# Kernel tuning notes

Hardware: AMD Instinct MI355X
Metric: run time of the kernel (lower is better)

## Reference

```python
import jax, jax.numpy as jnp
import numpy as np

B, T, C = 4, 2048, 1024
H = 16
D = C // H  # head_dim = 64
SCALE = D ** -0.5


def setup_inputs() -> dict:
    key = jax.random.key(0)
    ks = jax.random.split(key, 5)
    x = jax.random.normal(ks[0], (B, T, C), dtype=jnp.float32)
    w_qkv = jax.random.normal(ks[1], (3 * C, C), dtype=jnp.float32) * (C ** -0.5)
    b_qkv = jnp.zeros((3 * C,), dtype=jnp.float32)
    w_proj = jax.random.normal(ks[2], (C, C), dtype=jnp.float32) * (C ** -0.5)
    b_proj = jnp.zeros((C,), dtype=jnp.float32)
    return {"x": x, "w_qkv": w_qkv, "b_qkv": b_qkv, "w_proj": w_proj, "b_proj": b_proj}


def reference(x, w_qkv, b_qkv, w_proj, b_proj):
    b, t, c = x.shape
    # fused qkv projection (torch Linear: x @ W.T + b)
    qkv = x @ w_qkv.T + b_qkv                      # [B, T, 3C]
    q, k, v = jnp.split(qkv, 3, axis=2)
    # [B, T, C] -> [B, H, T, D]
    q = q.reshape(b, t, H, D).transpose(0, 2, 1, 3)
    k = k.reshape(b, t, H, D).transpose(0, 2, 1, 3)
    v = v.reshape(b, t, H, D).transpose(0, 2, 1, 3)
    att = jnp.einsum('bhqd,bhkd->bhqk', q, k) * SCALE
    causal = jnp.tril(jnp.ones((t, t), dtype=bool))  # True = keep
    att = jnp.where(causal, att, -jnp.inf)
    att = jax.nn.softmax(att, axis=-1)
    out = jnp.einsum('bhqk,bhkd->bhqd', att, v)
    out = out.transpose(0, 2, 1, 3).reshape(b, t, c)
    return out @ w_proj.T + b_proj
```

## Files before the change

### kernel.cpp

```cpp
#include <hip/hip_runtime.h>

typedef unsigned short u16;
typedef __attribute__((ext_vector_type(8))) short short8;
typedef __attribute__((ext_vector_type(4))) float f32x4;
typedef __attribute__((ext_vector_type(16))) float f32x16;
typedef __attribute__((ext_vector_type(2))) unsigned uint2v;
typedef __attribute__((ext_vector_type(4))) unsigned u32x4;

#define AS1 __attribute__((address_space(1)))
#define AS3 __attribute__((address_space(3)))

constexpr int Bn = 4, Tn = 2048, Cn = 1024, Hn = 16, Dn = 64;
constexpr float SCL_LOG2E = 0.125f * 1.44269504088896f;

__device__ __forceinline__ u16 f2bf(float f) {
  union { float f; unsigned u; } v; v.f = f;
  unsigned r = v.u + 0x7FFFu + ((v.u >> 16) & 1u);
  return (u16)(r >> 16);
}

__device__ __forceinline__ unsigned cvtpk_bf16(float a, float b) {
  unsigned r;
  asm("v_cvt_pk_bf16_f32 %0, %1, %2" : "=v"(r) : "v"(a), "v"(b));
  return r;
}

__global__ void cast_f32_to_bf16(const float* __restrict__ in, u16* __restrict__ out, int n4) {
  int i = blockIdx.x * 256 + threadIdx.x;
  if (i >= n4) return;
  float4 v = ((const float4*)in)[i];
  ushort4 o;
  o.x = f2bf(v.x); o.y = f2bf(v.y); o.z = f2bf(v.z); o.w = f2bf(v.w);
  ((ushort4*)out)[i] = o;
}

template <typename OT>
__global__ __launch_bounds__(512) void gemm8(
    const u16* __restrict__ A, const u16* __restrict__ Bm,
    const float* __restrict__ bias, OT* __restrict__ C,
    int M, int N, int K, int nbn, int qcols, float qscale)
{
  __shared__ u16 As[2][128 * 64];
  __shared__ u16 Bs[2][128 * 64];

  const int tid = threadIdx.x;
  const int lane = tid & 63;
  const int w = tid >> 6;
  const int wm = w >> 2, wn = w & 3;
  const int l15 = lane & 15, lg = lane >> 4;

  const int nwg = gridDim.x;
  const int wg = (blockIdx.x & 7) * (nwg >> 3) + (blockIdx.x >> 3);
  const int m0 = (wg / nbn) * 128;
  const int n0 = (wg % nbn) * 128;
  const int NT = K >> 6;

  const int wrow = wm * 64;
  const int wcol = wn * 32;

  f32x4 acc[4][2] = {};

  auto stage_A = [&](int tt) {
    if (tt >= NT) return;
    const int bu = tt & 1;
#pragma unroll
    for (int it = 0; it < 2; ++it) {
      const int c = it * 512 + tid;
      const int row = c >> 3;
      const int cs = (c & 7) ^ (row & 7);
      const u16* g = A + (size_t)(m0 + row) * K + tt * 64 + cs * 8;
      __builtin_amdgcn_global_load_lds((const AS1 void*)g,
          (AS3 void*)(&As[bu][c * 8]), 16, 0, 0);
    }
  };
  auto stage_B = [&](int tt) {
    if (tt >= NT) return;
    const int bu = tt & 1;
#pragma unroll
    for (int it = 0; it < 2; ++it) {
      const int c = it * 512 + tid;
      const int row = c >> 3;
      const int cs = (c & 7) ^ (row & 7);
      const u16* g = Bm + (size_t)(n0 + row) * K + tt * 64 + cs * 8;
      __builtin_amdgcn_global_load_lds((const AS1 void*)g,
          (AS3 void*)(&Bs[bu][c * 8]), 16, 0, 0);
    }
  };

  auto readA = [&](int bu, int mh, short8 (*a)[2]) {
#pragma unroll
    for (int i = 0; i < 2; ++i)
#pragma unroll
      for (int ks = 0; ks < 2; ++ks) {
        const int ra = wrow + (mh * 2 + i) * 16 + l15;
        a[i][ks] = *(const short8*)(&As[bu][ra * 64 + (((ks * 4 + lg) ^ (ra & 7)) << 3)]);
      }
  };
  auto readB = [&](int bu, int nh, short8 (*b)[2]) {
#pragma unroll
    for (int ks = 0; ks < 2; ++ks) {
      const int rb = wcol + nh * 16 + l15;
      b[0][ks] = *(const short8*)(&Bs[bu][rb * 64 + (((ks * 4 + lg) ^ (rb & 7)) << 3)]);
    }
  };
  auto mmaq = [&](int mh, int nh, short8 (*a)[2], short8 (*b)[2]) {
    __builtin_amdgcn_s_setprio(1);
#pragma unroll
    for (int i = 0; i < 2; ++i)
#pragma unroll
      for (int ks = 0; ks < 2; ++ks)
        acc[mh * 2 + i][nh] = __builtin_amdgcn_mfma_f32_16x16x32_bf16(
            a[i][ks], b[0][ks], acc[mh * 2 + i][nh], 0, 0, 0);
    __builtin_amdgcn_s_setprio(0);
  };

  stage_A(0);
  stage_B(0);
  stage_A(1);
  asm volatile("s_waitcnt vmcnt(2)" ::: "memory");
  __builtin_amdgcn_sched_barrier(0);
  __builtin_amdgcn_s_barrier();

  for (int t = 0; t < NT; ++t) {
    const int bu = t & 1;
    short8 a0[2][2], a1[2][2], b0[1][2], b1[1][2];
    readA(bu, 0, a0);
    readB(bu, 0, b0);
    stage_B(t + 1);
    __builtin_amdgcn_s_barrier();
    mmaq(0, 0, a0, b0);
    __builtin_amdgcn_s_barrier();
    readB(bu, 1, b1);
    __builtin_amdgcn_s_barrier();
    mmaq(0, 1, a0, b1);
    __builtin_amdgcn_s_barrier();
    readA(bu, 1, a1);
    __builtin_amdgcn_s_barrier();
    mmaq(1, 1, a1, b1);
    __builtin_amdgcn_s_barrier();
    stage_A(t + 2);
    __builtin_amdgcn_s_barrier();
    mmaq(1, 0, a1, b0);
    if (t + 2 < NT) {
      asm volatile("s_waitcnt vmcnt(2)" ::: "memory");
      __builtin_amdgcn_sched_barrier(0);
    } else if (t + 1 < NT) {
      asm volatile("s_waitcnt vmcnt(0)" ::: "memory");
      __builtin_amdgcn_sched_barrier(0);
    }
    __builtin_amdgcn_s_barrier();
  }

  __syncthreads();
  if constexpr (__is_same(OT, u16)) {
    u16* bounce = &As[0][0];
#pragma unroll
    for (int i = 0; i < 4; ++i)
#pragma unroll
      for (int j = 0; j < 2; ++j) {
        const int colg = n0 + wcol + j * 16 + l15;
        const float sc = (colg < qcols) ? qscale : 1.0f;
        const float bv = bias[colg];
#pragma unroll
        for (int r = 0; r < 4; ++r)
          bounce[(wrow + i * 16 + lg * 4 + r) * 128 + wcol + j * 16 + l15] =
              f2bf((acc[i][j][r] + bv) * sc);
      }
    __syncthreads();
#pragma unroll
    for (int s = 0; s < 4; ++s) {
      const int u = s * 512 + tid;
      const int row = u >> 4, col = (u & 15) * 8;
      *(short8*)(C + (size_t)(m0 + row) * N + n0 + col) =
          *(const short8*)(&bounce[row * 128 + col]);
    }
  } else {
    float* bounce = (float*)&As[0][0];
#pragma unroll
    for (int cch = 0; cch < 2; ++cch) {
      if (wm == cch) {
#pragma unroll
        for (int i = 0; i < 4; ++i)
#pragma unroll
          for (int j = 0; j < 2; ++j) {
            const int colg = n0 + wcol + j * 16 + l15;
            const float bv = bias[colg];
#pragma unroll
            for (int r = 0; r < 4; ++r)
              bounce[(i * 16 + lg * 4 + r) * 128 + wcol + j * 16 + l15] =
                  acc[i][j][r] + bv;
          }
      }
      __syncthreads();
#pragma unroll
      for (int s = 0; s < 4; ++s) {
        const int u = s * 512 + tid;
        const int row = u >> 5, col = (u & 31) * 4;
        *(f32x4*)((float*)C + (size_t)(m0 + cch * 64 + row) * N + n0 + col) =
            *(const f32x4*)(&bounce[row * 128 + col]);
      }
      __syncthreads();
    }
  }
}

__global__ __launch_bounds__(256) void transpose_v(
    const u16* __restrict__ qkv, u16* __restrict__ vt)
{
  __shared__ u16 tile[64][72];
  const int bh = blockIdx.x >> 5;
  const int tt = blockIdx.x & 31;
  const int b = bh >> 4;
  const int h = bh & 15;
  const int tid = threadIdx.x;
  const int trow = tid >> 2;
  const int dseg = tid & 3;

  const u16* src = qkv + (size_t)(b * Tn + tt * 64 + trow) * (3 * Cn) + 2 * Cn + h * Dn + dseg * 16;
  short8 v0 = *(const short8*)src;
  short8 v1 = *(const short8*)(src + 8);
#pragma unroll
  for (int e = 0; e < 8; ++e) {
    tile[dseg * 16 + e][trow] = (u16)v0[e];
    tile[dseg * 16 + 8 + e][trow] = (u16)v1[e];
  }
  __syncthreads();

  const int drow = tid >> 2;
  const int tseg = tid & 3;
  u16* dst = vt + (size_t)(bh * Dn + drow) * Tn + tt * 64 + tseg * 16;
  *(short8*)dst = *(const short8*)&tile[drow][tseg * 16];
  *(short8*)(dst + 8) = *(const short8*)&tile[drow][tseg * 16 + 8];
}

__global__ __launch_bounds__(256) void attn_kernel(
    const u16* __restrict__ qkv, const u16* __restrict__ vt, u16* __restrict__ att)
{
  __shared__ u16 Ks[3][64 * 64];
  __shared__ u16 Vs[3][64 * 64];
  const int tid = threadIdx.x;
  const int lane = tid & 63;
  const int w = tid >> 6;
  const int l31 = lane & 31;
  const int hi = lane >> 5;

  const int blk = blockIdx.x;
  const int qt = (Tn / 128 - 1) - (blk >> 6);
  const int bh = blk & 63;
  const int b = bh >> 4;
  const int h = bh & 15;
  const int q0w = qt * 128 + w * 32;
  const int rowbase = b * Tn;
  const int koff = Cn + h * Dn;
  const size_t vbase = (size_t)bh * Dn * Tn;
  const int nt = 2 * qt + 2;
  const int ntw = 2 * qt + 1 + (w >> 1);

  short8 qf[4];
  {
    const u16* qp = qkv + (size_t)(rowbase + q0w + l31) * (3 * Cn) + h * Dn + hi * 8;
#pragma unroll
    for (int sub = 0; sub < 4; ++sub) qf[sub] = *(const short8*)(qp + sub * 16);
  }

  float m_r = -1e30f, l_r = 0.f;
  f32x16 oacc[2] = {};

#define STAGE(buf, t_)                                                            \
  {                                                                               \
    const int kt_ = (t_) * 64;                                                    \
    _Pragma("unroll")                                                             \
    for (int it = 0; it < 2; ++it) {                                              \
      int c = it * 256 + tid;                                                     \
      int row = c >> 3;                                                           \
      int cs = (c & 7) ^ (row & 7);                                               \
      const u16* gk = qkv + (size_t)(rowbase + kt_ + row) * (3 * Cn) + koff + cs * 8; \
      __builtin_amdgcn_global_load_lds((const AS1 void*)gk, (AS3 void*)(&Ks[buf][c * 8]), 16, 0, 0); \
      const u16* gv = vt + vbase + (size_t)row * Tn + kt_ + cs * 8;               \
      __builtin_amdgcn_global_load_lds((const AS1 void*)gv, (AS3 void*)(&Vs[buf][c * 8]), 16, 0, 0); \
    }                                                                             \
  }

  STAGE(0, 0);
  STAGE(1, 1);
  asm volatile("s_waitcnt vmcnt(4)" ::: "memory");
  __builtin_amdgcn_sched_barrier(0);
  __builtin_amdgcn_s_barrier();
  __builtin_amdgcn_sched_barrier(0);

  for (int t = 0; t < nt; ++t) {
    const int cur = t % 3;
    if (t + 2 < nt) STAGE((t + 2) % 3, t + 2);
    if (t < ntw) {
      const int kt = t * 64;
      const u16* Kb = Ks[cur];
      const u16* Vb = Vs[cur];

      f32x16 s0 = {}, s1 = {};
#pragma unroll
      for (int sub = 0; sub < 4; ++sub) {
        const int ch = sub * 2 + hi;
        const int r0 = l31;
        short8 kf0 = *(const short8*)(Kb + r0 * 64 + ((ch ^ (r0 & 7)) << 3));
        s0 = __builtin_amdgcn_mfma_f32_32x32x16_bf16(kf0, qf[sub], s0, 0, 0, 0);
        const int r1 = 32 + l31;
        short8 kf1 = *(const short8*)(Kb + r1 * 64 + ((ch ^ (r1 & 7)) << 3));
        s1 = __builtin_amdgcn_mfma_f32_32x32x16_bf16(kf1, qf[sub], s1, 0, 0, 0);
      }

      if (kt + 63 > q0w) {
        const int qa = q0w + l31;
#pragma unroll
        for (int r = 0; r < 16; ++r) {
          const int k0 = kt + ((r & 3) + 8 * (r >> 2)) + 4 * hi;
          if (k0 > qa) s0[r] = -1e30f;
          if (k0 + 32 > qa) s1[r] = -1e30f;
        }
      }

      float mx = s0[0];
#pragma unroll
      for (int r = 1; r < 16; ++r) mx = fmaxf(mx, s0[r]);
#pragma unroll
      for (int r = 0; r < 16; ++r) mx = fmaxf(mx, s1[r]);
      mx = fmaxf(mx, __shfl_xor(mx, 32));

      if (__any(mx > m_r + 8.f)) {
        const float mnew = fmaxf(m_r, mx);
        const float a = __builtin_amdgcn_exp2f(m_r - mnew);
        m_r = mnew;
        l_r *= a;
#pragma unroll
        for (int r = 0; r < 16; ++r) { oacc[0][r] *= a; oacc[1][r] *= a; }
      }

      float ps = 0.f;
#pragma unroll
      for (int r = 0; r < 16; ++r) {
        s0[r] = __builtin_amdgcn_exp2f(s0[r] - m_r); ps += s0[r];
        s1[r] = __builtin_amdgcn_exp2f(s1[r] - m_r); ps += s1[r];
      }
      ps += __shfl_xor(ps, 32);
      l_r += ps;

      short8 pfr[4];
#pragma unroll
      for (int ks = 0; ks < 4; ++ks) {
        const f32x16& sv = (ks < 2) ? s0 : s1;
        const int base = (ks & 1) * 8;
        unsigned a0 = cvtpk_bf16(sv[base + 0], sv[base + 1]);
        unsigned a1 = cvtpk_bf16(sv[base + 2], sv[base + 3]);
        unsigned b0 = cvtpk_bf16(sv[base + 4], sv[base + 5]);
        unsigned b1 = cvtpk_bf16(sv[base + 6], sv[base + 7]);
        uint2v s_0 = __builtin_amdgcn_permlane32_swap(a0, b0, false, false);
        uint2v s_1 = __builtin_amdgcn_permlane32_swap(a1, b1, false, false);
        union { u32x4 u; short8 s; } cvt;
        cvt.u = (u32x4){s_0.x, s_1.x, s_0.y, s_1.y};
        pfr[ks] = cvt.s;
      }

#pragma unroll
      for (int j = 0; j < 2; ++j) {
        const int rv = j * 32 + l31;
        const int rsw = (rv & 7) << 3;
#pragma unroll
        for (int ks = 0; ks < 4; ++ks) {
          short8 vf = *(const short8*)(Vb + rv * 64 + (((ks * 2 + hi) << 3) ^ rsw));
          oacc[j] = __builtin_amdgcn_mfma_f32_32x32x16_bf16(vf, pfr[ks], oacc[j], 0, 0, 0);
        }
      }
    }
    if (t + 2 < nt)      asm volatile("s_waitcnt vmcnt(4)" ::: "memory");
    else if (t + 1 < nt) asm volatile("s_waitcnt vmcnt(0)" ::: "memory");
    __builtin_amdgcn_sched_barrier(0);
    __builtin_amdgcn_s_barrier();
    __builtin_amdgcn_sched_barrier(0);
  }

  {
    const float inv = __builtin_amdgcn_rcpf(l_r);
    u16* orow = att + (size_t)(rowbase + q0w + l31) * Cn + h * Dn + hi * 4;
#pragma unroll
    for (int j = 0; j < 2; ++j)
#pragma unroll
      for (int g = 0; g < 4; ++g) {
        ushort4 o;
#pragma unroll
        for (int c = 0; c < 4; ++c) o[c] = f2bf(oacc[j][g * 4 + c] * inv);
        *(ushort4*)(orow + j * 32 + g * 8) = o;
      }
  }
#undef STAGE
}

extern "C" void kernel_launch(void* const* d_in, const int* in_sizes, int n_in,
                              void* d_out, int out_size, void* d_ws, size_t ws_size,
                              hipStream_t stream) {
  const float* x      = (const float*)d_in[0];
  const float* w_qkv  = (const float*)d_in[1];
  const float* b_qkv  = (const float*)d_in[2];
  const float* w_proj = (const float*)d_in[3];
  const float* b_proj = (const float*)d_in[4];
  float* out = (float*)d_out;

  char* ws = (char*)d_ws;
  u16* x_bf     = (u16*)(ws);
  u16* wqkv_bf  = (u16*)(ws + 16777216);
  u16* wproj_bf = (u16*)(ws + 16777216 + 6291456);
  u16* qkv      = (u16*)(ws + 25165824);
  u16* att      = (u16*)(ws + 75497472);
  u16* vt       = x_bf;

  const int M = Bn * Tn;

  cast_f32_to_bf16<<<(M * Cn / 4 + 255) / 256, 256, 0, stream>>>(x, x_bf, M * Cn / 4);
  cast_f32_to_bf16<<<(3 * Cn * Cn / 4 + 255) / 256, 256, 0, stream>>>(w_qkv, wqkv_bf, 3 * Cn * Cn / 4);
  cast_f32_to_bf16<<<(Cn * Cn / 4 + 255) / 256, 256, 0, stream>>>(w_proj, wproj_bf, Cn * Cn / 4);

  gemm8<u16><<<1536, 512, 0, stream>>>(
      x_bf, wqkv_bf, b_qkv, qkv, M, 3 * Cn, Cn, 24, Cn, SCL_LOG2E);

  transpose_v<<<Bn * Hn * (Tn / 64), 256, 0, stream>>>(qkv, vt);

  attn_kernel<<<Bn * Hn * (Tn / 128), 256, 0, stream>>>(qkv, vt, att);

  gemm8<float><<<512, 512, 0, stream>>>(
      att, wproj_bf, b_proj, out, M, Cn, Cn, 8, 0, 1.0f);
}
```

Before: 174.2 us.

## Use 256x256-tile GEMM with ping-pong barrier schedule for QKV projection

Adds a new bf16 GEMM kernel with 256x256 output tiles (8 waves, each computing 128x64), double-buffered LDS staging through direct global-to-LDS loads, and an interleaved read/MFMA/stage schedule separated by workgroup barriers. The epilogue writes through an LDS bounce buffer to produce coalesced 16-byte row stores. The QKV projection now launches 384 of these larger tiles instead of 1536 128x128 tiles. The aim is higher operand reuse and less global traffic per FLOP. In exchange, 128 KB of LDS per block and a large accumulator set reduce occupancy, and with only 384 tiles the GPU's compute units may not be evenly loaded.

Result: slower. 181.6 us (+4.3%).

```diff
diff --git a/kernel.cpp b/kernel.cpp
--- a/kernel.cpp
+++ b/kernel.cpp
@@ -32,6 +32,156 @@
   ushort4 o;
   o.x = f2bf(v.x); o.y = f2bf(v.y); o.z = f2bf(v.z); o.w = f2bf(v.w);
   ((ushort4*)out)[i] = o;
+}
+
+__device__ __forceinline__ void store_out(u16* p, float v) { *p = f2bf(v); }
+__device__ __forceinline__ void store_out(float* p, float v) { *p = v; }
+
+__global__ __launch_bounds__(512, 2) void gemm256(
+    const u16* __restrict__ A, const u16* __restrict__ Bm,
+    const float* __restrict__ bias, u16* __restrict__ C,
+    int M, int N, int K, int nbn, int qcols, float qscale)
+{
+  __shared__ u16 As[2][256 * 64];
+  __shared__ u16 Bs[2][256 * 64];
+
+  const int tid = threadIdx.x;
+  const int lane = tid & 63;
+  const int w = tid >> 6;
+  const int wm = w >> 2, wn = w & 3;
+  const int l15 = lane & 15, lg = lane >> 4;
+
+  const int nwg = gridDim.x;
+  const int wg = (blockIdx.x & 7) * (nwg >> 3) + (blockIdx.x >> 3);
+  const int m0 = (wg / nbn) * 256;
+  const int n0 = (wg % nbn) * 256;
+  const int NT = K >> 6;
+
+  f32x4 acc[8][4] = {};
+
+  auto stage_A = [&](int tt, int h) {
+    if (tt >= NT) return;
+    const int bu = tt & 1;
+#pragma unroll
+    for (int it = 0; it < 2; ++it) {
+      const int c = it * 512 + tid;
+      const int row = c >> 3;
+      const int cs = (c & 7) ^ (row & 7);
+      const u16* g = A + (size_t)(m0 + h * 128 + row) * K + tt * 64 + cs * 8;
+      __builtin_amdgcn_global_load_lds((const AS1 void*)g,
+          (AS3 void*)(&As[bu][(h * 128 + row) * 64 + (c & 7) * 8]), 16, 0, 0);
+    }
+  };
+  auto stage_B = [&](int tt, int h) {
+    if (tt >= NT) return;
+    const int bu = tt & 1;
+#pragma unroll
+    for (int it = 0; it < 2; ++it) {
+      const int c = it * 512 + tid;
+      const int row = c >> 3;
+      const int cs = (c & 7) ^ (row & 7);
+      const u16* g = Bm + (size_t)(n0 + h * 128 + row) * K + tt * 64 + cs * 8;
+      __builtin_amdgcn_global_load_lds((const AS1 void*)g,
+          (AS3 void*)(&Bs[bu][(h * 128 + row) * 64 + (c & 7) * 8]), 16, 0, 0);
+    }
+  };
+
+  auto readA = [&](int bu, int mh, short8 (*a)[2]) {
+#pragma unroll
+    for (int i = 0; i < 4; ++i)
+#pragma unroll
+      for (int ks = 0; ks < 2; ++ks) {
+        const int ra = wm * 128 + mh * 64 + i * 16 + l15;
+        a[i][ks] = *(const short8*)(&As[bu][ra * 64 + (((ks * 4 + lg) ^ (ra & 7)) << 3)]);
+      }
+  };
+  auto readB = [&](int bu, int nh2, short8 (*b)[2]) {
+#pragma unroll
+    for (int j = 0; j < 2; ++j)
+#pragma unroll
+      for (int ks = 0; ks < 2; ++ks) {
+        const int rb = wn * 64 + nh2 * 32 + j * 16 + l15;
+        b[j][ks] = *(const short8*)(&Bs[bu][rb * 64 + (((ks * 4 + lg) ^ (rb & 7)) << 3)]);
+      }
+  };
+  auto mmaq = [&](int mh, int nh2, short8 (*a)[2], short8 (*b)[2]) {
+    __builtin_amdgcn_s_setprio(1);
+#pragma unroll
+    for (int i = 0; i < 4; ++i)
+#pragma unroll
+      for (int j = 0; j < 2; ++j)
+#pragma unroll
+        for (int ks = 0; ks < 2; ++ks)
+          acc[mh * 4 + i][nh2 * 2 + j] = __builtin_amdgcn_mfma_f32_16x16x32_bf16(
+              a[i][ks], b[j][ks], acc[mh * 4 + i][nh2 * 2 + j], 0, 0, 0);
+    __builtin_amdgcn_s_setprio(0);
+  };
+
+  stage_A(0, 0); stage_A(0, 1); stage_B(0, 0); stage_B(0, 1);
+  stage_A(1, 0); stage_A(1, 1); stage_B(1, 0);
+  asm volatile("s_waitcnt vmcnt(6)" ::: "memory");
+  __builtin_amdgcn_sched_barrier(0);
+  __builtin_amdgcn_s_barrier();
+
+  for (int t = 0; t < NT; ++t) {
+    const int bu = t & 1;
+    short8 a0[4][2], a1[4][2], b0[2][2], b1[2][2];
+    readA(bu, 0, a0);
+    readB(bu, 0, b0);
+    stage_B(t + 1, 1);
+    __builtin_amdgcn_s_barrier();
+    mmaq(0, 0, a0, b0);
+    __builtin_amdgcn_s_barrier();
+    readA(bu, 1, a1);
+    __builtin_amdgcn_s_barrier();
+    mmaq(1, 0, a1, b0);
+    __builtin_amdgcn_s_barrier();
+    readB(bu, 1, b1);
+    stage_A(t + 2, 0);
+    __builtin_amdgcn_s_barrier();
+    mmaq(1, 1, a1, b1);
+    __builtin_amdgcn_s_barrier();
+    stage_A(t + 2, 1);
+    stage_B(t + 2, 0);
+    __builtin_amdgcn_s_barrier();
+    mmaq(0, 1, a0, b1);
+    if (t + 2 < NT) {
+      asm volatile("s_waitcnt vmcnt(6)" ::: "memory");
+      __builtin_amdgcn_sched_barrier(0);
+    } else if (t + 1 < NT) {
+      asm volatile("s_waitcnt vmcnt(0)" ::: "memory");
+      __builtin_amdgcn_sched_barrier(0);
+    }
+    __builtin_amdgcn_s_barrier();
+  }
+
+  u16* bounce = &As[0][0];
+#pragma unroll 1
+  for (int cch = 0; cch < 2; ++cch) {
+    __builtin_amdgcn_s_barrier();
+    if (wm == cch) {
+#pragma unroll
+      for (int i = 0; i < 8; ++i)
+#pragma unroll
+        for (int j = 0; j < 4; ++j) {
+          const int colg = n0 + wn * 64 + j * 16 + l15;
+          const float sc = (colg < qcols) ? qscale : 1.0f;
+          const float bv = bias[colg];
+#pragma unroll
+          for (int r = 0; r < 4; ++r)
+            bounce[(i * 16 + lg * 4 + r) * 256 + wn * 64 + j * 16 + l15] =
+                f2bf((acc[i][j][r] + bv) * sc);
+        }
+    }
+    __builtin_amdgcn_s_barrier();
+#pragma unroll
+    for (int s = 0; s < 8; ++s) {
+      const int u = s * 512 + tid;
+      const int row = u >> 5, col = (u & 31) * 8;
+      *(short8*)(C + (size_t)(m0 + cch * 128 + row) * N + n0 + col) =
+          *(const short8*)(&bounce[row * 256 + col]);
+    }
+  }
 }
 
 template <typename OT>
@@ -417,8 +567,8 @@
   cast_f32_to_bf16<<<(3 * Cn * Cn / 4 + 255) / 256, 256, 0, stream>>>(w_qkv, wqkv_bf, 3 * Cn * Cn / 4);
   cast_f32_to_bf16<<<(Cn * Cn / 4 + 255) / 256, 256, 0, stream>>>(w_proj, wproj_bf, Cn * Cn / 4);
 
-  gemm8<u16><<<1536, 512, 0, stream>>>(
-      x_bf, wqkv_bf, b_qkv, qkv, M, 3 * Cn, Cn, 24, Cn, SCL_LOG2E);
+  gemm256<<<384, 512, 0, stream>>>(
+      x_bf, wqkv_bf, b_qkv, qkv, M, 3 * Cn, Cn, 12, Cn, SCL_LOG2E);
 
   transpose_v<<<Bn * Hn * (Tn / 64), 256, 0, stream>>>(qkv, vt);
 
```
